# Kernel optimization log

Measured on AMD Instinct MI355X. Metric: run time of the kernel, lower is better.

Reference implementation:

```python
import jax, jax.numpy as jnp
import numpy as np

B, T, C, H = 8, 2048, 1024, 64  # batch, context_length, embedding_dim, head_size


def setup_inputs() -> dict:
    key = jax.random.key(0)
    kx, kq, kk, kv = jax.random.split(key, 4)
    s = C ** -0.5  # linear-init-like scale
    return {
        "x": jax.random.normal(kx, (B, T, C), dtype=jnp.float32),
        "Wq": jax.random.normal(kq, (C, H), dtype=jnp.float32) * s,
        "Wk": jax.random.normal(kk, (C, H), dtype=jnp.float32) * s,
        "Wv": jax.random.normal(kv, (C, H), dtype=jnp.float32) * s,
    }


def reference(x, Wq, Wk, Wv):
    Bx, Tx, _ = x.shape
    q = jnp.einsum('btc,ch->bth', x, Wq)
    k = jnp.einsum('btc,ch->bth', x, Wk)
    v = jnp.einsum('btc,ch->bth', x, Wv)
    scale = k.shape[-1] ** -0.5
    scores = jnp.einsum('bth,bsh->bts', q, k) * scale  # [B, T, T]
    causal = jnp.tril(jnp.ones((Tx, Tx), dtype=bool))
    scores = jnp.where(causal, scores, -jnp.inf)
    weights = jax.nn.softmax(scores, axis=-1)
    # dropout is identity in eval mode
    out = jnp.einsum('bts,bsh->bth', weights, v)  # [B, T, H]
    return out
```

## Files before the change

kernel.cpp:

```cpp
#include <hip/hip_runtime.h>
#include <hip/hip_bf16.h>

#define BB 8
#define TT 2048
#define CC 1024
#define HH 64

typedef float f32x4 __attribute__((ext_vector_type(4)));
typedef float f32x16 __attribute__((ext_vector_type(16)));
typedef short s16x8 __attribute__((ext_vector_type(8)));

static __device__ __forceinline__ unsigned short f2bf(float f) {
    unsigned int u = __float_as_uint(f);
    u = (u + 0x7FFFu + ((u >> 16) & 1u)) >> 16;
    return (unsigned short)u;
}

static __device__ __forceinline__ unsigned cvt_pk_bf16(float lo, float hi) {
    unsigned r;
    asm("v_cvt_pk_bf16_f32 %0, %1, %2" : "=v"(r) : "v"(lo), "v"(hi));
    return r;
}

__global__ __launch_bounds__(256) void wt_kernel(
    const float* __restrict__ Wq, const float* __restrict__ Wk,
    const float* __restrict__ Wv, unsigned short* __restrict__ wTf) {
    const int e8 = blockIdx.x * 256 + threadIdx.x;
    const int lane = e8 & 63;
    const int s = (e8 >> 6) & 31;
    const int n16 = e8 >> 11;
    const int sel = n16 >> 2;
    const float* W = (sel == 0) ? Wq : ((sel == 1) ? Wk : Wv);
    const int h = ((n16 & 3) << 4) + (lane & 15);
    const int cb = s * 32 + ((lane >> 4) << 3);
    s16x8 v;
#pragma unroll
    for (int j = 0; j < 8; ++j) v[j] = (short)f2bf(W[(size_t)(cb + j) * HH + h]);
    *reinterpret_cast<s16x8*>(&wTf[(size_t)e8 * 8]) = v;
}

__global__ __launch_bounds__(256, 2) void qkv_kernel(
    const float* __restrict__ x, const unsigned short* __restrict__ wTf,
    unsigned short* __restrict__ Qf, unsigned short* __restrict__ Kf,
    unsigned short* __restrict__ Vf) {
    __shared__ unsigned short xt[32 * 1024];
    const int tid = threadIdx.x;
    const int wn = tid >> 6, lane = tid & 63;
    const int lo = lane & 15, hi = lane >> 4;
    const int rb = blockIdx.x * 32;

#pragma unroll
    for (int i = 0; i < 16; ++i) {
        const int gid = tid + 256 * i;
        const int row = gid >> 7, g = gid & 127;
        const float* src = &x[(size_t)(rb + row) * CC + g * 8];
        const f32x4 f0 = *reinterpret_cast<const f32x4*>(src);
        const f32x4 f1 = *reinterpret_cast<const f32x4*>(src + 4);
        s16x8 w;
        w[0] = (short)f2bf(f0[0]); w[1] = (short)f2bf(f0[1]);
        w[2] = (short)f2bf(f0[2]); w[3] = (short)f2bf(f0[3]);
        w[4] = (short)f2bf(f1[0]); w[5] = (short)f2bf(f1[1]);
        w[6] = (short)f2bf(f1[2]); w[7] = (short)f2bf(f1[3]);
        *reinterpret_cast<s16x8*>(&xt[row * 1024 + (g ^ (row & 7)) * 8]) = w;
    }
    __syncthreads();

    f32x4 acc[2][3];
#pragma unroll
    for (int m = 0; m < 2; ++m)
#pragma unroll
        for (int n = 0; n < 3; ++n) acc[m][n] = (f32x4){0.f, 0.f, 0.f, 0.f};

    s16x8 bv[4][3];
#define BLOAD(SET, SLOT)                                                       \
    {                                                                          \
        _Pragma("unroll")                                                      \
        for (int n = 0; n < 3; ++n)                                            \
            bv[SET][n] = *reinterpret_cast<const s16x8*>(                      \
                &wTf[(((size_t)(wn * 3 + n) * 32 + (SLOT)) * 64 + lane) * 8]); \
    }
    BLOAD(0, 0)
    BLOAD(1, 1)
    BLOAD(2, 2)

    const int sw = lo & 7;
#pragma unroll
    for (int slot = 0; slot < 32; ++slot) {
        if (slot + 3 < 32) BLOAD((slot + 3) & 3, slot + 3)
        const int gr = slot * 4 + hi;
        const s16x8 a0 = *reinterpret_cast<const s16x8*>(
            &xt[lo * 1024 + (gr ^ sw) * 8]);
        const s16x8 a1 = *reinterpret_cast<const s16x8*>(
            &xt[(16 + lo) * 1024 + (gr ^ sw) * 8]);
#pragma unroll
        for (int n = 0; n < 3; ++n) {
            acc[0][n] = __builtin_amdgcn_mfma_f32_16x16x32_bf16(a0, bv[slot & 3][n], acc[0][n], 0, 0, 0);
            acc[1][n] = __builtin_amdgcn_mfma_f32_16x16x32_bf16(a1, bv[slot & 3][n], acc[1][n], 0, 0, 0);
        }
    }
#undef BLOAD

    __syncthreads();
    unsigned short* fr = xt;
#pragma unroll
    for (int n = 0; n < 3; ++n) {
        const int n16 = wn * 3 + n;
        const int sel = n16 >> 2;
#pragma unroll
        for (int m = 0; m < 2; ++m) {
#pragma unroll
            for (int r = 0; r < 4; ++r) {
                const int tok31 = m * 16 + 4 * hi + r;
                const unsigned short bvv = f2bf(acc[m][n][r]);
                if (sel == 0) {
                    const int s = n16, half = (lo >> 3) & 1, j = lo & 7;
                    fr[(s * 64 + half * 32 + tok31) * 8 + j] = bvv;
                } else if (sel == 1) {
                    const int s = n16 - 4, half = (lo >> 3) & 1, j = lo & 7;
                    fr[2048 + (s * 64 + half * 32 + tok31) * 8 + j] = bvv;
                } else {
                    const int h = (n16 - 8) * 16 + lo;
                    const int mt = h >> 5;
                    const int s2 = tok31 >> 4, hf = (tok31 >> 3) & 1, jj = tok31 & 7;
                    fr[4096 + ((mt * 2 + s2) * 64 + hf * 32 + (h & 31)) * 8 + jj] = bvv;
                }
            }
        }
    }
    __syncthreads();
    const int b_ = rb >> 11;
    const int tile = (rb & (TT - 1)) >> 5;
    const size_t tb = ((size_t)b_ * 64 + tile) * 2048;
#pragma unroll
    for (int i = 0; i < 3; ++i) {
        const int g = tid + 256 * i;
        const int buf = g >> 8;
        const int off = g & 255;
        const s16x8 val = *reinterpret_cast<const s16x8*>(&fr[buf * 2048 + off * 8]);
        unsigned short* dst = (buf == 0) ? Qf : ((buf == 1) ? Kf : Vf);
        *reinterpret_cast<s16x8*>(&dst[tb + off * 8]) = val;
    }
}

__global__ __launch_bounds__(512, 4) void attn_kernel(
    const unsigned short* __restrict__ Qf, const unsigned short* __restrict__ Kf,
    const unsigned short* __restrict__ Vf, float* __restrict__ out) {
    __shared__ __align__(16) char smem[33792 + 2048];
    float (*OfL)[64][33] = reinterpret_cast<float(*)[64][33]>(smem);
    float (*Mm)[32] = reinterpret_cast<float(*)[32]>(smem + 33792);
    float (*Ml)[32] = reinterpret_cast<float(*)[32]>(smem + 33792 + 1024);

    const int tid = threadIdx.x;
    const int wv = tid >> 6, lane = tid & 63;
    const int q = lane & 31, half = lane >> 5;
    const int b = blockIdx.x & 7;
    const int qt = 63 - (blockIdx.x >> 3);
    const int qbase = qt * 32;
    const float CEXP = 0.125f * 1.44269504f;

    const unsigned short* qp = &Qf[(((size_t)b * 64 + qt) * 256 + lane) * 8];
    s16x8 qf[4];
#pragma unroll
    for (int s = 0; s < 4; ++s) qf[s] = *reinterpret_cast<const s16x8*>(qp + s * 512);

    f32x16 oA, oB;
#pragma unroll
    for (int r = 0; r < 16; ++r) { oA[r] = 0.f; oB[r] = 0.f; }
    float m = -1e30f, l = 0.f;

    for (int t = wv; t <= qt; t += 8) {
        const unsigned short* vp = &Vf[(((size_t)b * 64 + t) * 256 + lane) * 8];
        s16x8 vf[4];
#pragma unroll
        for (int i = 0; i < 4; ++i)
            vf[i] = *reinterpret_cast<const s16x8*>(vp + i * 512);
        const unsigned short* kp = &Kf[(((size_t)b * 64 + t) * 256 + lane) * 8];
        f32x16 sa;
#pragma unroll
        for (int r = 0; r < 16; ++r) sa[r] = 0.f;
#pragma unroll
        for (int s = 0; s < 4; ++s) {
            const s16x8 kf = *reinterpret_cast<const s16x8*>(kp + s * 512);
            sa = __builtin_amdgcn_mfma_f32_32x32x16_bf16(kf, qf[s], sa, 0, 0, 0);
        }
        if (t == qt) {
#pragma unroll
            for (int r = 0; r < 16; ++r) {
                const int key = 4 * half + (r & 3) + 8 * (r >> 2);
                if (key > q) sa[r] = -1e30f;
            }
        }
        float pmax = sa[0];
#pragma unroll
        for (int r = 1; r < 16; ++r) pmax = fmaxf(pmax, sa[r]);
        pmax = fmaxf(pmax, __shfl_xor(pmax, 32));
        if (!__all(pmax <= m + 64.f)) {
            const float mnew = fmaxf(m, pmax);
            const float alpha = exp2f((m - mnew) * CEXP);
            l *= alpha;
#pragma unroll
            for (int r = 0; r < 16; ++r) { oA[r] *= alpha; oB[r] *= alpha; }
            m = mnew;
        }
        float rs = 0.f;
#pragma unroll
        for (int r = 0; r < 16; ++r) {
            const float p = exp2f((sa[r] - m) * CEXP);
            sa[r] = p;
            rs += p;
        }
        l += rs + __shfl_xor(rs, 32);
        unsigned d[8];
#pragma unroll
        for (int i = 0; i < 8; ++i) d[i] = cvt_pk_bf16(sa[2 * i], sa[2 * i + 1]);
        const unsigned snd0 = half ? d[0] : d[2];
        const unsigned snd1 = half ? d[1] : d[3];
        const unsigned snd2 = half ? d[4] : d[6];
        const unsigned snd3 = half ? d[5] : d[7];
        const unsigned rcv0 = __shfl_xor(snd0, 32);
        const unsigned rcv1 = __shfl_xor(snd1, 32);
        const unsigned rcv2 = __shfl_xor(snd2, 32);
        const unsigned rcv3 = __shfl_xor(snd3, 32);
        union { unsigned u[4]; s16x8 v; } f0, f1;
        f0.u[0] = half ? rcv0 : d[0];
        f0.u[1] = half ? rcv1 : d[1];
        f0.u[2] = half ? d[2] : rcv0;
        f0.u[3] = half ? d[3] : rcv1;
        f1.u[0] = half ? rcv2 : d[4];
        f1.u[1] = half ? rcv3 : d[5];
        f1.u[2] = half ? d[6] : rcv2;
        f1.u[3] = half ? d[7] : rcv3;
        oA = __builtin_amdgcn_mfma_f32_32x32x16_bf16(vf[0], f0.v, oA, 0, 0, 0);
        oB = __builtin_amdgcn_mfma_f32_32x32x16_bf16(vf[2], f0.v, oB, 0, 0, 0);
        oA = __builtin_amdgcn_mfma_f32_32x32x16_bf16(vf[1], f1.v, oA, 0, 0, 0);
        oB = __builtin_amdgcn_mfma_f32_32x32x16_bf16(vf[3], f1.v, oB, 0, 0, 0);
    }

#define PUBLISH(slot)                                                      \
    {                                                                      \
        _Pragma("unroll")                                                  \
        for (int r = 0; r < 16; ++r) {                                     \
            const int h0 = (r & 3) + 8 * (r >> 2) + 4 * half;              \
            OfL[slot][h0][q] = oA[r];                                      \
            OfL[slot][h0 + 32][q] = oB[r];                                 \
        }                                                                  \
    }
#define MERGE(slot, srcw)                                                  \
    {                                                                      \
        const float mb = Mm[srcw][q], lb = Ml[srcw][q];                    \
        const float M = fmaxf(m, mb);                                      \
        const float wa = exp2f((m - M) * CEXP);                            \
        const float wb = exp2f((mb - M) * CEXP);                           \
        _Pragma("unroll")                                                  \
        for (int r = 0; r < 16; ++r) {                                     \
            const int h0 = (r & 3) + 8 * (r >> 2) + 4 * half;              \
            oA[r] = oA[r] * wa + OfL[slot][h0][q] * wb;                    \
            oB[r] = oB[r] * wa + OfL[slot][h0 + 32][q] * wb;               \
        }                                                                  \
        l = l * wa + lb * wb;                                              \
        m = M;                                                             \
    }

    if (lane < 32) { Mm[wv][q] = m; Ml[wv][q] = l; }
    if (wv >= 4) PUBLISH(wv - 4);
    __syncthreads();
    if (wv < 4) MERGE(wv, wv + 4);
    __syncthreads();
    if (wv == 2 || wv == 3) {
        PUBLISH(wv - 2);
        if (lane < 32) { Mm[wv][q] = m; Ml[wv][q] = l; }
    }
    __syncthreads();
    if (wv < 2) MERGE(wv, wv + 2);
    __syncthreads();
    if (wv == 1) {
        PUBLISH(1);
        if (lane < 32) { Mm[1][q] = m; Ml[1][q] = l; }
    }
    __syncthreads();
    if (wv == 0) {
        MERGE(1, 1);
        const float inv = 1.f / l;
#pragma unroll
        for (int r = 0; r < 16; ++r) {
            const int h0 = (r & 3) + 8 * (r >> 2) + 4 * half;
            OfL[0][h0][q] = oA[r] * inv;
            OfL[0][h0 + 32][q] = oB[r] * inv;
        }
    }
    __syncthreads();
#pragma unroll
    for (int i = 0; i < 4; ++i) {
        const int idx = tid + 512 * i;
        const int h = idx & 63, q2 = idx >> 6;
        out[((size_t)b * TT + qbase + q2) * HH + h] = OfL[0][h][q2];
    }
#undef PUBLISH
#undef MERGE
}

extern "C" void kernel_launch(void* const* d_in, const int* in_sizes, int n_in,
                              void* d_out, int out_size, void* d_ws, size_t ws_size,
                              hipStream_t stream) {
    (void)in_sizes; (void)n_in; (void)out_size; (void)ws_size;
    const float* x  = (const float*)d_in[0];
    const float* Wq = (const float*)d_in[1];
    const float* Wk = (const float*)d_in[2];
    const float* Wv = (const float*)d_in[3];
    float* out = (float*)d_out;

    char* ws = (char*)d_ws;
    unsigned short* wTf = (unsigned short*)ws;
    unsigned short* Qf  = (unsigned short*)(ws + 393216);
    unsigned short* Kf  = (unsigned short*)(ws + 393216 + 2097152);
    unsigned short* Vf  = (unsigned short*)(ws + 393216 + 4194304);

    wt_kernel<<<96, 256, 0, stream>>>(Wq, Wk, Wv, wTf);
    qkv_kernel<<<512, 256, 0, stream>>>(x, wTf, Qf, Kf, Vf);
    attn_kernel<<<512, 512, 0, stream>>>(Qf, Kf, Vf, out);
}
```

Before: 45.06 us.

## Load x directly into MFMA registers, drop 64KB LDS staging in QKV kernel

The QKV projection kernel no longer stages a 32x1024 bf16 tile of x in shared memory. Each wave now reads its fp32 x fragments straight from global memory and converts them with packed bf16 conversion instructions. LDS shrinks to a small output buffer and the launch bound rises to 4 blocks per CU, aiming for more occupancy and fewer barriers. In exchange, every one of the four waves reads the same x rows from global memory, relying on the cache, and the explicit prefetch pipeline for the weight fragments is removed.

```diff
diff --git a/kernel.cpp b/kernel.cpp
--- a/kernel.cpp
+++ b/kernel.cpp
@@ -39,31 +39,18 @@
     *reinterpret_cast<s16x8*>(&wTf[(size_t)e8 * 8]) = v;
 }
 
-__global__ __launch_bounds__(256, 2) void qkv_kernel(
+__global__ __launch_bounds__(256, 4) void qkv_kernel(
     const float* __restrict__ x, const unsigned short* __restrict__ wTf,
     unsigned short* __restrict__ Qf, unsigned short* __restrict__ Kf,
     unsigned short* __restrict__ Vf) {
-    __shared__ unsigned short xt[32 * 1024];
+    __shared__ unsigned short fr[6144];
     const int tid = threadIdx.x;
     const int wn = tid >> 6, lane = tid & 63;
     const int lo = lane & 15, hi = lane >> 4;
     const int rb = blockIdx.x * 32;
 
-#pragma unroll
-    for (int i = 0; i < 16; ++i) {
-        const int gid = tid + 256 * i;
-        const int row = gid >> 7, g = gid & 127;
-        const float* src = &x[(size_t)(rb + row) * CC + g * 8];
-        const f32x4 f0 = *reinterpret_cast<const f32x4*>(src);
-        const f32x4 f1 = *reinterpret_cast<const f32x4*>(src + 4);
-        s16x8 w;
-        w[0] = (short)f2bf(f0[0]); w[1] = (short)f2bf(f0[1]);
-        w[2] = (short)f2bf(f0[2]); w[3] = (short)f2bf(f0[3]);
-        w[4] = (short)f2bf(f1[0]); w[5] = (short)f2bf(f1[1]);
-        w[6] = (short)f2bf(f1[2]); w[7] = (short)f2bf(f1[3]);
-        *reinterpret_cast<s16x8*>(&xt[row * 1024 + (g ^ (row & 7)) * 8]) = w;
-    }
-    __syncthreads();
+    const float* xr0 = &x[(size_t)(rb + lo) * CC + hi * 8];
+    const float* xr1 = &x[(size_t)(rb + 16 + lo) * CC + hi * 8];
 
     f32x4 acc[2][3];
 #pragma unroll
@@ -71,37 +58,34 @@
 #pragma unroll
         for (int n = 0; n < 3; ++n) acc[m][n] = (f32x4){0.f, 0.f, 0.f, 0.f};
 
-    s16x8 bv[4][3];
-#define BLOAD(SET, SLOT)                                                       \
-    {                                                                          \
-        _Pragma("unroll")                                                      \
-        for (int n = 0; n < 3; ++n)                                            \
-            bv[SET][n] = *reinterpret_cast<const s16x8*>(                      \
-                &wTf[(((size_t)(wn * 3 + n) * 32 + (SLOT)) * 64 + lane) * 8]); \
-    }
-    BLOAD(0, 0)
-    BLOAD(1, 1)
-    BLOAD(2, 2)
-
-    const int sw = lo & 7;
-#pragma unroll
+#pragma unroll 8
     for (int slot = 0; slot < 32; ++slot) {
-        if (slot + 3 < 32) BLOAD((slot + 3) & 3, slot + 3)
-        const int gr = slot * 4 + hi;
-        const s16x8 a0 = *reinterpret_cast<const s16x8*>(
-            &xt[lo * 1024 + (gr ^ sw) * 8]);
-        const s16x8 a1 = *reinterpret_cast<const s16x8*>(
-            &xt[(16 + lo) * 1024 + (gr ^ sw) * 8]);
+        const int ko = slot * 32;
+        const f32x4 a00 = *reinterpret_cast<const f32x4*>(xr0 + ko);
+        const f32x4 a01 = *reinterpret_cast<const f32x4*>(xr0 + ko + 4);
+        const f32x4 a10 = *reinterpret_cast<const f32x4*>(xr1 + ko);
+        const f32x4 a11 = *reinterpret_cast<const f32x4*>(xr1 + ko + 4);
+        s16x8 b[3];
+#pragma unroll
+        for (int n = 0; n < 3; ++n)
+            b[n] = *reinterpret_cast<const s16x8*>(
+                &wTf[(((size_t)(wn * 3 + n) * 32 + slot) * 64 + lane) * 8]);
+        union { unsigned u[4]; s16x8 v; } a0, a1;
+        a0.u[0] = cvt_pk_bf16(a00[0], a00[1]);
+        a0.u[1] = cvt_pk_bf16(a00[2], a00[3]);
+        a0.u[2] = cvt_pk_bf16(a01[0], a01[1]);
+        a0.u[3] = cvt_pk_bf16(a01[2], a01[3]);
+        a1.u[0] = cvt_pk_bf16(a10[0], a10[1]);
+        a1.u[1] = cvt_pk_bf16(a10[2], a10[3]);
+        a1.u[2] = cvt_pk_bf16(a11[0], a11[1]);
+        a1.u[3] = cvt_pk_bf16(a11[2], a11[3]);
 #pragma unroll
         for (int n = 0; n < 3; ++n) {
-            acc[0][n] = __builtin_amdgcn_mfma_f32_16x16x32_bf16(a0, bv[slot & 3][n], acc[0][n], 0, 0, 0);
-            acc[1][n] = __builtin_amdgcn_mfma_f32_16x16x32_bf16(a1, bv[slot & 3][n], acc[1][n], 0, 0, 0);
-        }
-    }
-#undef BLOAD
-
-    __syncthreads();
-    unsigned short* fr = xt;
+            acc[0][n] = __builtin_amdgcn_mfma_f32_16x16x32_bf16(a0.v, b[n], acc[0][n], 0, 0, 0);
+            acc[1][n] = __builtin_amdgcn_mfma_f32_16x16x32_bf16(a1.v, b[n], acc[1][n], 0, 0, 0);
+        }
+    }
+
 #pragma unroll
     for (int n = 0; n < 3; ++n) {
         const int n16 = wn * 3 + n;
```

New measurement: 82.31 us. +82.6%, slower.

## Restructure QKV projection to 64-row tiles with 12 waves and register-resident weights

Applied to the files above, without the earlier changes.

The QKV projection kernel now handles 64 tokens per block with 768 threads (12 waves), each wave owning one 16-column slice of the fused QKV weight. Each wave preloads its whole weight slice (32 slots) into registers up front instead of streaming it with a 3-deep prefetch. Weight traffic per token is halved and fewer blocks are launched. In exchange the block uses 128KB of LDS and many vector registers (32 s16x8 per thread), which limits occupancy and lengthens the x-staging phase.

```diff
diff --git a/kernel.cpp b/kernel.cpp
--- a/kernel.cpp
+++ b/kernel.cpp
@@ -39,106 +39,97 @@
     *reinterpret_cast<s16x8*>(&wTf[(size_t)e8 * 8]) = v;
 }
 
-__global__ __launch_bounds__(256, 2) void qkv_kernel(
+__global__ __launch_bounds__(768, 3) void qkv_kernel(
     const float* __restrict__ x, const unsigned short* __restrict__ wTf,
     unsigned short* __restrict__ Qf, unsigned short* __restrict__ Kf,
     unsigned short* __restrict__ Vf) {
-    __shared__ unsigned short xt[32 * 1024];
+    __shared__ unsigned short xt[64 * 1024];
     const int tid = threadIdx.x;
     const int wn = tid >> 6, lane = tid & 63;
     const int lo = lane & 15, hi = lane >> 4;
-    const int rb = blockIdx.x * 32;
-
-#pragma unroll
-    for (int i = 0; i < 16; ++i) {
-        const int gid = tid + 256 * i;
-        const int row = gid >> 7, g = gid & 127;
-        const float* src = &x[(size_t)(rb + row) * CC + g * 8];
-        const f32x4 f0 = *reinterpret_cast<const f32x4*>(src);
-        const f32x4 f1 = *reinterpret_cast<const f32x4*>(src + 4);
-        s16x8 w;
-        w[0] = (short)f2bf(f0[0]); w[1] = (short)f2bf(f0[1]);
-        w[2] = (short)f2bf(f0[2]); w[3] = (short)f2bf(f0[3]);
-        w[4] = (short)f2bf(f1[0]); w[5] = (short)f2bf(f1[1]);
-        w[6] = (short)f2bf(f1[2]); w[7] = (short)f2bf(f1[3]);
-        *reinterpret_cast<s16x8*>(&xt[row * 1024 + (g ^ (row & 7)) * 8]) = w;
-    }
-    __syncthreads();
-
-    f32x4 acc[2][3];
-#pragma unroll
-    for (int m = 0; m < 2; ++m)
-#pragma unroll
-        for (int n = 0; n < 3; ++n) acc[m][n] = (f32x4){0.f, 0.f, 0.f, 0.f};
-
-    s16x8 bv[4][3];
-#define BLOAD(SET, SLOT)                                                       \
-    {                                                                          \
-        _Pragma("unroll")                                                      \
-        for (int n = 0; n < 3; ++n)                                            \
-            bv[SET][n] = *reinterpret_cast<const s16x8*>(                      \
-                &wTf[(((size_t)(wn * 3 + n) * 32 + (SLOT)) * 64 + lane) * 8]); \
-    }
-    BLOAD(0, 0)
-    BLOAD(1, 1)
-    BLOAD(2, 2)
+    const int rb = blockIdx.x * 64;
+
+    s16x8 bp[32];
+#pragma unroll
+    for (int slot = 0; slot < 32; ++slot)
+        bp[slot] = *reinterpret_cast<const s16x8*>(
+            &wTf[(((size_t)wn * 32 + slot) * 64 + lane) * 8]);
+
+#pragma unroll
+    for (int i = 0; i < 11; ++i) {
+        const int g = tid + 768 * i;
+        if (g < 8192) {
+            const int row = g >> 7, c8 = g & 127;
+            const float* src = &x[(size_t)(rb + row) * CC + c8 * 8];
+            const f32x4 f0 = *reinterpret_cast<const f32x4*>(src);
+            const f32x4 f1 = *reinterpret_cast<const f32x4*>(src + 4);
+            s16x8 w;
+            w[0] = (short)f2bf(f0[0]); w[1] = (short)f2bf(f0[1]);
+            w[2] = (short)f2bf(f0[2]); w[3] = (short)f2bf(f0[3]);
+            w[4] = (short)f2bf(f1[0]); w[5] = (short)f2bf(f1[1]);
+            w[6] = (short)f2bf(f1[2]); w[7] = (short)f2bf(f1[3]);
+            *reinterpret_cast<s16x8*>(&xt[row * 1024 + ((c8 ^ (row & 7)) * 8)]) = w;
+        }
+    }
+    __syncthreads();
+
+    f32x4 acc[4];
+#pragma unroll
+    for (int m = 0; m < 4; ++m) acc[m] = (f32x4){0.f, 0.f, 0.f, 0.f};
 
     const int sw = lo & 7;
 #pragma unroll
     for (int slot = 0; slot < 32; ++slot) {
-        if (slot + 3 < 32) BLOAD((slot + 3) & 3, slot + 3)
         const int gr = slot * 4 + hi;
-        const s16x8 a0 = *reinterpret_cast<const s16x8*>(
-            &xt[lo * 1024 + (gr ^ sw) * 8]);
-        const s16x8 a1 = *reinterpret_cast<const s16x8*>(
-            &xt[(16 + lo) * 1024 + (gr ^ sw) * 8]);
-#pragma unroll
-        for (int n = 0; n < 3; ++n) {
-            acc[0][n] = __builtin_amdgcn_mfma_f32_16x16x32_bf16(a0, bv[slot & 3][n], acc[0][n], 0, 0, 0);
-            acc[1][n] = __builtin_amdgcn_mfma_f32_16x16x32_bf16(a1, bv[slot & 3][n], acc[1][n], 0, 0, 0);
-        }
-    }
-#undef BLOAD
+#pragma unroll
+        for (int m = 0; m < 4; ++m) {
+            const int row = m * 16 + lo;
+            const s16x8 a = *reinterpret_cast<const s16x8*>(
+                &xt[row * 1024 + ((gr ^ sw) * 8)]);
+            acc[m] = __builtin_amdgcn_mfma_f32_16x16x32_bf16(a, bp[slot], acc[m], 0, 0, 0);
+        }
+    }
 
     __syncthreads();
     unsigned short* fr = xt;
-#pragma unroll
-    for (int n = 0; n < 3; ++n) {
-        const int n16 = wn * 3 + n;
-        const int sel = n16 >> 2;
-#pragma unroll
-        for (int m = 0; m < 2; ++m) {
-#pragma unroll
-            for (int r = 0; r < 4; ++r) {
-                const int tok31 = m * 16 + 4 * hi + r;
-                const unsigned short bvv = f2bf(acc[m][n][r]);
-                if (sel == 0) {
-                    const int s = n16, half = (lo >> 3) & 1, j = lo & 7;
-                    fr[(s * 64 + half * 32 + tok31) * 8 + j] = bvv;
-                } else if (sel == 1) {
-                    const int s = n16 - 4, half = (lo >> 3) & 1, j = lo & 7;
-                    fr[2048 + (s * 64 + half * 32 + tok31) * 8 + j] = bvv;
-                } else {
-                    const int h = (n16 - 8) * 16 + lo;
-                    const int mt = h >> 5;
-                    const int s2 = tok31 >> 4, hf = (tok31 >> 3) & 1, jj = tok31 & 7;
-                    fr[4096 + ((mt * 2 + s2) * 64 + hf * 32 + (h & 31)) * 8 + jj] = bvv;
-                }
+    const int sel = wn >> 2;
+#pragma unroll
+    for (int m = 0; m < 4; ++m) {
+        const int tib = m >> 1;
+        const int ib = tib * 6144;
+#pragma unroll
+        for (int r = 0; r < 4; ++r) {
+            const int tok31 = (m & 1) * 16 + 4 * hi + r;
+            const unsigned short bvv = f2bf(acc[m][r]);
+            if (sel == 0) {
+                const int s = wn, half = (lo >> 3) & 1, j = lo & 7;
+                fr[ib + (s * 64 + half * 32 + tok31) * 8 + j] = bvv;
+            } else if (sel == 1) {
+                const int s = wn - 4, half = (lo >> 3) & 1, j = lo & 7;
+                fr[ib + 2048 + (s * 64 + half * 32 + tok31) * 8 + j] = bvv;
+            } else {
+                const int h = (wn - 8) * 16 + lo;
+                const int mt = h >> 5;
+                const int s2 = tok31 >> 4, hf = (tok31 >> 3) & 1, jj = tok31 & 7;
+                fr[ib + 4096 + ((mt * 2 + s2) * 64 + hf * 32 + (h & 31)) * 8 + jj] = bvv;
             }
         }
     }
     __syncthreads();
     const int b_ = rb >> 11;
-    const int tile = (rb & (TT - 1)) >> 5;
-    const size_t tb = ((size_t)b_ * 64 + tile) * 2048;
-#pragma unroll
-    for (int i = 0; i < 3; ++i) {
-        const int g = tid + 256 * i;
-        const int buf = g >> 8;
-        const int off = g & 255;
-        const s16x8 val = *reinterpret_cast<const s16x8*>(&fr[buf * 2048 + off * 8]);
+    const int tile0 = (rb & (TT - 1)) >> 5;
+#pragma unroll
+    for (int i = 0; i < 2; ++i) {
+        const int g = tid + 768 * i;
+        const int tib = (g >= 768) ? 1 : 0;
+        const int rem = g - tib * 768;
+        const int buf = rem >> 8;
+        const int off = rem & 255;
+        const s16x8 val = *reinterpret_cast<const s16x8*>(
+            &fr[tib * 6144 + buf * 2048 + off * 8]);
         unsigned short* dst = (buf == 0) ? Qf : ((buf == 1) ? Kf : Vf);
-        *reinterpret_cast<s16x8*>(&dst[tb + off * 8]) = val;
+        *reinterpret_cast<s16x8*>(
+            &dst[((size_t)b_ * 64 + tile0 + tib) * 2048 + off * 8]) = val;
     }
 }
 
@@ -316,6 +307,6 @@
     unsigned short* Vf  = (unsigned short*)(ws + 393216 + 4194304);
 
     wt_kernel<<<96, 256, 0, stream>>>(Wq, Wk, Wv, wTf);
-    qkv_kernel<<<512, 256, 0, stream>>>(x, wTf, Qf, Kf, Vf);
+    qkv_kernel<<<256, 768, 0, stream>>>(x, wTf, Qf, Kf, Vf);
     attn_kernel<<<512, 512, 0, stream>>>(Qf, Kf, Vf, out);
 }
```

Result: faster. 43.97 us (-2.4%).
